# Optimization experiments

Measured on AMD Instinct MI355X. Metric: run time of the kernel, lower is better.

The kernel has to match this reference:

```python
import jax, jax.numpy as jnp
import numpy as np

B, S, F_IN, H, P2 = 64, 64, 2048, 512, 20  # batch, seq_len, input_size, hidden, 2*num_prototype


def setup_inputs() -> dict:
    key = jax.random.key(0)
    ks = jax.random.split(key, 16)
    sc = 0.02
    inp = {
        "v_feat": jax.random.normal(ks[0], (B, S, F_IN), jnp.float32),
        "category": jax.random.randint(ks[1], (B,), 0, 3, jnp.int64),
        "W_enc": jax.random.normal(ks[2], (F_IN, H), jnp.float32) * sc,
        "b_enc": jnp.zeros((H,), jnp.float32),
        # gate order along last axis: input, forget, output, memory(g)
        "Wx": jax.random.normal(ks[3], (H, 4 * H), jnp.float32) * sc,
        "bx": jnp.zeros((4 * H,), jnp.float32),
        "Wh": jax.random.normal(ks[4], (H, 4 * H), jnp.float32) * sc,
        "bh": jnp.zeros((4 * H,), jnp.float32),
        "cat_emb": jax.random.normal(ks[5], (3, H), jnp.float32) * sc,
        "W_dec": jax.random.normal(ks[6], (H, 1), jnp.float32) * sc,
        "b_dec": jnp.zeros((1,), jnp.float32),
        "prototype": jax.random.uniform(ks[7], (P2, F_IN), jnp.float32),
        "W_dd": jax.random.normal(ks[8], (P2 * S, 1), jnp.float32) * sc,
        "b_dd": jnp.zeros((1,), jnp.float32),
        "W_gate": jax.random.normal(ks[9], (F_IN, 1), jnp.float32) * sc,
        "b_gate": jnp.zeros((1,), jnp.float32),
    }
    return inp


def _forward(v_feat, category, W_enc, b_enc, Wx, bx, Wh, bh, cat_emb,
             W_dec, b_dec, prototype, W_dd, b_dd, W_gate, b_gate):
    batch, seq, feat = v_feat.shape
    # encoder + category fusion
    fuse = jax.nn.relu(jnp.einsum('bsf,fh->bsh', v_feat, W_enc) + b_enc)
    fuse = fuse + cat_emb[category][:, None, :]

    # fused-gate LSTM over time (note: original cell has NO tanh on cell in h = o*c)
    x_gates = jnp.einsum('bsh,hg->sbg', fuse, Wx) + (bx + bh)  # precompute input GEMM

    def step(carry, xg):
        h, c = carry
        gates = xg + h @ Wh
        i, f, o, g = jnp.split(gates, 4, axis=-1)
        i, f, o = jax.nn.sigmoid(i), jax.nn.sigmoid(f), jax.nn.sigmoid(o)
        g = jnp.tanh(g)
        c = f * c + i * g
        h = o * c
        return (h, c), None

    h0 = jnp.zeros((batch, Wh.shape[0]), fuse.dtype)
    (h, c), _ = jax.lax.scan(step, (h0, h0), x_gates)

    # dropout p=0.5 omitted (deterministic eval reference)
    output = jax.nn.sigmoid(h @ W_dec + b_dec)  # [B,1]

    # prototype distances: [B,S,2P]
    diff = v_feat[:, :, None, :] - prototype[None, None, :, :]
    dist = jnp.sum(diff * diff, axis=-1)
    dist_feat = jnp.log((dist + 1.0) / (dist + 1e-8))
    dist_pred = jax.nn.sigmoid(dist_feat.reshape(batch, -1) @ W_dd + b_dd)
    gate = jax.nn.sigmoid(jnp.mean(v_feat, axis=1) @ W_gate + b_gate)
    return output * gate + dist_pred * (1.0 - gate)


def reference(v_feat, category, W_enc, b_enc, Wx, bx, Wh, bh, cat_emb,
              W_dec, b_dec, prototype, W_dd, b_dd, W_gate, b_gate):
    return _forward(v_feat, category, W_enc, b_enc, Wx, bx, Wh, bh, cat_emb,
                    W_dec, b_dec, prototype, W_dd, b_dd, W_gate, b_gate)
```

## Files before the change

kernel.cpp:

```cpp
#include <hip/hip_runtime.h>
#include <cstdint>
#include <cstddef>


typedef __attribute__((ext_vector_type(8))) short short8;
typedef __attribute__((ext_vector_type(4))) float f32x4;
typedef unsigned long long ull;

__device__ __forceinline__ ushort f2bf(float x) {
    uint32_t u = __float_as_uint(x);
    return (ushort)((u + 0x7FFF + ((u >> 16) & 1)) >> 16);
}
__device__ __forceinline__ float bf2f(ushort u) {
    return __uint_as_float(((uint32_t)u) << 16);
}
__device__ __forceinline__ float sigm(float x) { return 1.f / (1.f + expf(-x)); }
__device__ __forceinline__ float tanh_fast(float x) { return 2.f / (1.f + expf(-2.f * x)) - 1.f; }

__global__ __launch_bounds__(256) void k_prep(
    const float* __restrict__ v_feat, const float* __restrict__ proto,
    const float* __restrict__ bx, const float* __restrict__ bh,
    const float* __restrict__ W_enc, const float* __restrict__ Wx,
    const float* __restrict__ Wh, const float* __restrict__ W_gate,
    ushort* __restrict__ v_bf16, ushort* __restrict__ proto_bf,
    float* __restrict__ bxh, ushort* __restrict__ Wenc_t,
    ushort* __restrict__ Wx_t, ushort* __restrict__ Whr,
    float* __restrict__ n2, float* __restrict__ gpart, float* __restrict__ p2,
    ushort* __restrict__ hbuf, int* __restrict__ flags, int* __restrict__ dd_done,
    int* __restrict__ xgf)
{
    __shared__ float ts[32][33];
    const int blk = blockIdx.x;
    const int tid = threadIdx.x;

    if (blk < 4096) {
        const int bs = blk;
        const float* vr = v_feat + (size_t)bs * 2048;
        float4 x0 = ((const float4*)vr)[tid];
        float4 x1 = ((const float4*)vr)[tid + 256];
        float4 w0 = ((const float4*)W_gate)[tid];
        float4 w1 = ((const float4*)W_gate)[tid + 256];
        ushort4 o0, o1;
        o0.x = f2bf(x0.x); o0.y = f2bf(x0.y); o0.z = f2bf(x0.z); o0.w = f2bf(x0.w);
        o1.x = f2bf(x1.x); o1.y = f2bf(x1.y); o1.z = f2bf(x1.z); o1.w = f2bf(x1.w);
        ((ushort4*)v_bf16)[(size_t)bs * 512 + tid] = o0;
        ((ushort4*)v_bf16)[(size_t)bs * 512 + tid + 256] = o1;
        float a = x0.x * x0.x + x0.y * x0.y + x0.z * x0.z + x0.w * x0.w
                + x1.x * x1.x + x1.y * x1.y + x1.z * x1.z + x1.w * x1.w;
        float g = x0.x * w0.x + x0.y * w0.y + x0.z * w0.z + x0.w * w0.w
                + x1.x * w1.x + x1.y * w1.y + x1.z * w1.z + x1.w * w1.w;
        const int lane = tid & 63, w = tid >> 6;
#pragma unroll
        for (int o = 32; o > 0; o >>= 1) { a += __shfl_down(a, o); g += __shfl_down(g, o); }
        if (lane == 0) { ts[0][w] = a; ts[1][w] = g; }
        __syncthreads();
        if (tid == 0) {
            n2[bs]    = ts[0][0] + ts[0][1] + ts[0][2] + ts[0][3];
            gpart[bs] = ts[1][0] + ts[1][1] + ts[1][2] + ts[1][3];
        }
    } else if (blk < 4136) {
        int i = (blk - 4096) * 256 + tid;
        float4 v = ((const float4*)proto)[i];
        ushort4 o;
        o.x = f2bf(v.x); o.y = f2bf(v.y); o.z = f2bf(v.z); o.w = f2bf(v.w);
        ((ushort4*)proto_bf)[i] = o;
    } else if (blk < 4148) {
        int row = 20 + (blk - 4136);
        ushort4 z = {0, 0, 0, 0};
        ((ushort4*)(proto_bf + (size_t)row * 2048))[tid * 2] = z;
        ((ushort4*)(proto_bf + (size_t)row * 2048))[tid * 2 + 1] = z;
    } else if (blk < 4156) {
        int n = (blk - 4148) * 256 + tid;
        int np = ((n & 511) << 2) | (n >> 9);
        bxh[np] = bx[n] + bh[n];
    } else if (blk < 7228) {
        const float* in;
        ushort* outp;
        int R, C, remap, t;
        if (blk < 5180)      { in = W_enc; outp = Wenc_t; R = 2048; C = 512;  remap = 0; t = blk - 4156; }
        else if (blk < 6204) { in = Wx;    outp = Wx_t;   R = 512;  C = 2048; remap = 1; t = blk - 5180; }
        else                 { in = Wh;    outp = Whr;    R = 512;  C = 2048; remap = 1; t = blk - 6204; }
        int tpr = C / 32;
        int cx = t % tpr, cy = t / tpr;
        int r0 = cy * 32, c0 = cx * 32;
        int rr = tid >> 3, cc = (tid & 7) * 4;
        float4 v = *(const float4*)(in + (size_t)(r0 + rr) * C + c0 + cc);
        ts[rr][cc + 0] = v.x; ts[rr][cc + 1] = v.y; ts[rr][cc + 2] = v.z; ts[rr][cc + 3] = v.w;
        __syncthreads();
        ushort4 o;
        o.x = f2bf(ts[cc + 0][rr]);
        o.y = f2bf(ts[cc + 1][rr]);
        o.z = f2bf(ts[cc + 2][rr]);
        o.w = f2bf(ts[cc + 3][rr]);
        int n = c0 + rr;
        int np = remap ? (((n & 511) << 2) | (n >> 9)) : n;
        *(ushort4*)(outp + (size_t)np * R + r0 + cc) = o;
    } else if (blk == 7228) {
        const int lane = tid & 63, w = tid >> 6;
        for (int p = w; p < 20; p += 4) {
            const float* pr = proto + (size_t)p * 2048;
            float a = 0.f;
#pragma unroll
            for (int i = 0; i < 8; ++i) {
                float4 x = ((const float4*)pr)[i * 64 + lane];
                a += x.x * x.x + x.y * x.y + x.z * x.z + x.w * x.w;
            }
#pragma unroll
            for (int o = 32; o > 0; o >>= 1) a += __shfl_down(a, o);
            if (lane == 0) p2[p] = a;
        }
        if (tid == 0) *dd_done = 0;
    } else if (blk < 7261) {
        ((ull*)hbuf)[(blk - 7229) * 256 + tid] = 0ULL;
    } else {
        for (int i = tid; i < 2048; i += 256) flags[i] = 0;
        for (int i = tid; i < 512; i += 256) xgf[i] = 0;
    }
}

__global__ __launch_bounds__(256) void k_mid(
    const ushort* __restrict__ A, const ushort* __restrict__ Bt,
    const float* __restrict__ bias0,
    const float* __restrict__ cat_emb, const int* __restrict__ category,
    ushort* __restrict__ C,
    const ushort* __restrict__ proto_bf, float* __restrict__ dots)
{
    __shared__ ushort As[64][40];
    __shared__ ushort Bs[128][40];
    const int tid = threadIdx.x;
    const int lane = tid & 63, w = tid >> 6;
    const int quad = lane >> 4, l16 = lane & 15;
    const int blk = blockIdx.x;

    if (blk >= 256) {
        const int r0 = (blk - 256) * 64 + w * 16;
        f32x4 acc[2] = {};
        const ushort* arow = A + (size_t)(r0 + l16) * 2048 + quad * 8;
        const ushort* b0p = proto_bf + (size_t)l16 * 2048 + quad * 8;
        const ushort* b1p = proto_bf + (size_t)(16 + l16) * 2048 + quad * 8;
#pragma unroll 8
        for (int kk = 0; kk < 64; ++kk) {
            short8 af = *(const short8*)(arow + kk * 32);
            short8 bf0 = *(const short8*)(b0p + kk * 32);
            short8 bf1 = *(const short8*)(b1p + kk * 32);
            acc[0] = __builtin_amdgcn_mfma_f32_16x16x32_bf16(af, bf0, acc[0], 0, 0, 0);
            acc[1] = __builtin_amdgcn_mfma_f32_16x16x32_bf16(af, bf1, acc[1], 0, 0, 0);
        }
#pragma unroll
        for (int t = 0; t < 2; ++t)
#pragma unroll
            for (int r = 0; r < 4; ++r)
                dots[(size_t)(r0 + quad * 4 + r) * 32 + t * 16 + l16] = acc[t][r];
        return;
    }

    const int m0 = (blk >> 2) * 64, n0 = (blk & 3) * 128;
    const int wm = (w & 1) * 32, wn = (w >> 1) * 64;
    const int K = 2048;

    f32x4 acc[2][4] = {};
    const int lr = tid >> 2;
    const int lc = (tid & 3) * 8;

    for (int k0 = 0; k0 < K; k0 += 32) {
        uint4 a0 = *(const uint4*)(A + (size_t)(m0 + lr) * K + k0 + lc);
        uint4 b0 = *(const uint4*)(Bt + (size_t)(n0 + lr) * K + k0 + lc);
        uint4 b1 = *(const uint4*)(Bt + (size_t)(n0 + 64 + lr) * K + k0 + lc);
        __syncthreads();
        *(uint4*)&As[lr][lc] = a0;
        *(uint4*)&Bs[lr][lc] = b0;
        *(uint4*)&Bs[64 + lr][lc] = b1;
        __syncthreads();
        short8 af[2], bf[4];
#pragma unroll
        for (int i = 0; i < 2; ++i) af[i] = *(const short8*)&As[wm + i * 16 + l16][quad * 8];
#pragma unroll
        for (int j = 0; j < 4; ++j) bf[j] = *(const short8*)&Bs[wn + j * 16 + l16][quad * 8];
#pragma unroll
        for (int i = 0; i < 2; ++i)
#pragma unroll
            for (int j = 0; j < 4; ++j)
                acc[i][j] = __builtin_amdgcn_mfma_f32_16x16x32_bf16(af[i], bf[j], acc[i][j], 0, 0, 0);
    }

#pragma unroll
    for (int i = 0; i < 2; ++i) {
        int mbase = m0 + wm + i * 16 + quad * 4;
#pragma unroll
        for (int r = 0; r < 4; ++r) {
            int m = mbase + r;
            const float* ce = cat_emb + category[m >> 6] * 512;
#pragma unroll
            for (int j = 0; j < 4; ++j) {
                int n = n0 + wn + j * 16 + l16;
                float v = fmaxf(acc[i][j][r] + bias0[n], 0.f) + ce[n];
                C[(size_t)m * 512 + n] = f2bf(v);
            }
        }
    }
}

__global__ __launch_bounds__(512, 2) void k_lstm_persist(
    ushort* __restrict__ xg,
    const ushort* __restrict__ fuse,
    const ushort* __restrict__ Wx_t,
    const float* __restrict__ bxh,
    int* __restrict__ xgf,
    const ushort* __restrict__ Whr,
    ushort* __restrict__ hbuf,
    int* __restrict__ flags,
    const float* __restrict__ W_dec, const float* __restrict__ b_dec,
    const float* __restrict__ b_dd, const float* __restrict__ b_gate,
    const float* __restrict__ dots, const float* __restrict__ n2,
    const float* __restrict__ p2, const float* __restrict__ W_dd,
    const float* __restrict__ gpart,
    float* __restrict__ dd_logit, float* __restrict__ g_logit,
    int* __restrict__ dd_done,
    float* __restrict__ out)
{
    __shared__ __align__(16) ushort hin_s[16 * 520];
    __shared__ __align__(16) ushort hstage[512];
    __shared__ float fred[8][64];
    __shared__ __align__(16) ushort As[128][40];
    __shared__ __align__(16) ushort Bs[128][40];

    const int tid = threadIdx.x;
    const int lane = tid & 63, wv = tid >> 6;
    const int quad = lane >> 4, l16 = lane & 15;
    const int bn = blockIdx.x;

    if (bn >= 320) {
        const int b = bn - 320;
        if (tid < 64) {
            float gp = gpart[b * 64 + tid];
#pragma unroll
            for (int o = 32; o > 0; o >>= 1) gp += __shfl_down(gp, o);
            if (tid == 0)
                __hip_atomic_store(&g_logit[b], gp, __ATOMIC_RELAXED, __HIP_MEMORY_SCOPE_AGENT);
        }
        float acc = 0.f;
        for (int u = tid; u < 1280; u += 512) {
            int s = u / 20, p = u - s * 20;
            int bs = b * 64 + s;
            float d = n2[bs] - 2.f * dots[(size_t)bs * 32 + p] + p2[p];
            acc += logf((d + 1.0f) / (d + 1e-8f)) * W_dd[s * 20 + p];
        }
#pragma unroll
        for (int o = 32; o > 0; o >>= 1) acc += __shfl_down(acc, o);
        if (lane == 0) fred[wv][0] = acc;
        __syncthreads();
        if (tid == 0) {
            float t = 0.f;
#pragma unroll
            for (int p = 0; p < 8; ++p) t += fred[p][0];
            __hip_atomic_store(&dd_logit[b], t, __ATOMIC_RELAXED, __HIP_MEMORY_SCOPE_AGENT);
            __hip_atomic_fetch_add(dd_done, 1, __ATOMIC_RELEASE, __HIP_MEMORY_SCOPE_AGENT);
        }
        return;
    }

    if (bn >= 64) {
        const int g = bn - 64;
        const int nc = g & 15;
        const int n0 = nc * 128;
        const int lrA = tid >> 2;
        const int lcA = (tid & 3) * 8;
        const int w8 = tid >> 6;
        const int wm8 = (w8 & 3) * 32, wn8 = (w8 >> 2) * 64;

#pragma unroll
        for (int ph = 0; ph < 2; ++ph) {
            const int mt = (ph ? 16 : 0) + (g >> 4);
            const int m0 = mt * 128;
            f32x4 acc[2][4] = {};
            for (int k0 = 0; k0 < 512; k0 += 32) {
                int ma = m0 + lrA;
                int fr = ((ma & 63) << 6) | (ma >> 6);
                uint4 a0 = *(const uint4*)(fuse + (size_t)fr * 512 + k0 + lcA);
                uint4 b0 = *(const uint4*)(Wx_t + (size_t)(n0 + lrA) * 512 + k0 + lcA);
                __syncthreads();
                *(uint4*)&As[lrA][lcA] = a0;
                *(uint4*)&Bs[lrA][lcA] = b0;
                __syncthreads();
                short8 af[2], bf[4];
#pragma unroll
                for (int i = 0; i < 2; ++i) af[i] = *(const short8*)&As[wm8 + i * 16 + l16][quad * 8];
#pragma unroll
                for (int j = 0; j < 4; ++j) bf[j] = *(const short8*)&Bs[wn8 + j * 16 + l16][quad * 8];
#pragma unroll
                for (int i = 0; i < 2; ++i)
#pragma unroll
                    for (int j = 0; j < 4; ++j)
                        acc[i][j] = __builtin_amdgcn_mfma_f32_16x16x32_bf16(af[i], bf[j], acc[i][j], 0, 0, 0);
            }
            float bb[4];
#pragma unroll
            for (int j = 0; j < 4; ++j) bb[j] = bxh[n0 + wn8 + j * 16 + l16];
#pragma unroll
            for (int i = 0; i < 2; ++i) {
                int mbase = m0 + wm8 + i * 16 + quad * 4;
#pragma unroll
                for (int r = 0; r < 4; ++r) {
                    ushort* crow = xg + (size_t)(mbase + r) * 2048;
#pragma unroll
                    for (int j = 0; j < 4; ++j)
                        crow[n0 + wn8 + j * 16 + l16] = f2bf(acc[i][j][r] + bb[j]);
                }
            }
            asm volatile("s_waitcnt vmcnt(0)" ::: "memory");
            __syncthreads();
            if (tid == 0)
                __hip_atomic_store(&xgf[mt * 16 + nc], 1, __ATOMIC_RELAXED,
                                   __HIP_MEMORY_SCOPE_AGENT);
        }
        return;
    }

    const int i = bn & 15;
    const int j = bn >> 4;
    const int uloc = wv * 4 + quad;

    short8 wfrag[16];
#pragma unroll
    for (int kc = 0; kc < 16; ++kc)
        wfrag[kc] = *(const short8*)(Whr +
            (size_t)(i * 128 + wv * 16 + l16) * 512 + kc * 32 + quad * 8);

    float c = 0.f;

    for (int s = 0; s < 64; ++s) {
        if (s > 0) {
            if (tid < 16) {
                const int* f = flags + (j * 16 + tid) * 32;
                while (__hip_atomic_load(f, __ATOMIC_RELAXED,
                                         __HIP_MEMORY_SCOPE_AGENT) < s) {}
            } else if (tid == 16) {
                const int xi = (s >> 1) * 16 + i;
                while (__hip_atomic_load(&xgf[xi], __ATOMIC_RELAXED,
                                         __HIP_MEMORY_SCOPE_AGENT) == 0) {}
            }
            __builtin_amdgcn_s_barrier();
            asm volatile("" ::: "memory");
        } else {
            if (tid == 0) {
                while (__hip_atomic_load(&xgf[i], __ATOMIC_RELAXED,
                                         __HIP_MEMORY_SCOPE_AGENT) == 0) {}
            }
            __builtin_amdgcn_s_barrier();
            asm volatile("" ::: "memory");
        }

        const ushort* xp = xg + (size_t)(s * 64 + j * 16 + l16) * 2048
                              + i * 128 + wv * 16 + quad * 4;
        ushort4 xa = *(const ushort4*)xp;

        const ushort* hin = hbuf + (size_t)s * 32768 + j * 8192;
        ushort* hout = hbuf + (size_t)(s + 1) * 32768 + j * 8192;

        {
            int r0 = wv * 2;
            __builtin_amdgcn_global_load_lds(
                (const __attribute__((address_space(1))) void*)(hin + (size_t)r0 * 512 + lane * 8),
                (__attribute__((address_space(3))) void*)(hin_s + r0 * 520),
                16, 0, 0);
            __builtin_amdgcn_global_load_lds(
                (const __attribute__((address_space(1))) void*)(hin + (size_t)(r0 + 1) * 512 + lane * 8),
                (__attribute__((address_space(3))) void*)(hin_s + (r0 + 1) * 520),
                16, 0, 0);
        }
        asm volatile("s_waitcnt vmcnt(0)" ::: "memory");
        __builtin_amdgcn_s_barrier();
        asm volatile("" ::: "memory");

        f32x4 aA = {bf2f(xa.x), bf2f(xa.y), bf2f(xa.z), bf2f(xa.w)};
        f32x4 aB = {};
#pragma unroll
        for (int kc = 0; kc < 16; kc += 2) {
            short8 h0 = *(const short8*)(hin_s + l16 * 520 + kc * 32 + quad * 8);
            short8 h1 = *(const short8*)(hin_s + l16 * 520 + (kc + 1) * 32 + quad * 8);
            aA = __builtin_amdgcn_mfma_f32_16x16x32_bf16(wfrag[kc], h0, aA, 0, 0, 0);
            aB = __builtin_amdgcn_mfma_f32_16x16x32_bf16(wfrag[kc + 1], h1, aB, 0, 0, 0);
        }

        float gi = sigm(aA[0] + aB[0]);
        float gf = sigm(aA[1] + aB[1]);
        float go = sigm(aA[2] + aB[2]);
        float gg = tanh_fast(aA[3] + aB[3]);
        c = gf * c + gi * gg;
        hstage[l16 * 32 + uloc] = f2bf(go * c);

        asm volatile("s_waitcnt lgkmcnt(0)" ::: "memory");
        __builtin_amdgcn_s_barrier();
        asm volatile("" ::: "memory");

        if (tid < 128) {
            int r = tid >> 3, ch = tid & 7;
            __hip_atomic_store((ull*)(hout + (size_t)r * 512 + i * 32) + ch,
                               ((const ull*)hstage)[tid],
                               __ATOMIC_RELAXED, __HIP_MEMORY_SCOPE_AGENT);
        }
        __syncthreads();
        if (tid == 0)
            __hip_atomic_store(&flags[bn * 32], s + 1, __ATOMIC_RELAXED,
                               __HIP_MEMORY_SCOPE_AGENT);
    }

    if (bn == 0) {
        if (tid < 64) {
            while (__hip_atomic_load(&flags[tid * 32], __ATOMIC_RELAXED,
                                     __HIP_MEMORY_SCOPE_AGENT) < 64) {}
        }
        __syncthreads();
        asm volatile("" ::: "memory");
        const ushort* hb64 = hbuf + (size_t)64 * 32768;
        int b = tid & 63, part = tid >> 6;
        const ushort* row = hb64 + (size_t)(b >> 4) * 8192 + (b & 15) * 512;
        float acc = 0.f;
#pragma unroll
        for (int g8 = 0; g8 < 8; ++g8) {
            const ushort* hp = row + part * 64 + g8 * 8;
            const float* wd = W_dec + part * 64 + g8 * 8;
#pragma unroll
            for (int half = 0; half < 2; ++half) {
                ull u = *(const ull*)(hp + half * 4);
                acc += bf2f((ushort)u) * wd[half * 4]
                     + bf2f((ushort)(u >> 16)) * wd[half * 4 + 1]
                     + bf2f((ushort)(u >> 32)) * wd[half * 4 + 2]
                     + bf2f((ushort)(u >> 48)) * wd[half * 4 + 3];
            }
        }
        fred[part][b] = acc;
        __syncthreads();
        if (tid == 0) {
            while (__hip_atomic_load(dd_done, __ATOMIC_RELAXED,
                                     __HIP_MEMORY_SCOPE_AGENT) < 64) {}
        }
        __syncthreads();
        asm volatile("" ::: "memory");
        if (tid < 64) {
            float a = 0.f;
#pragma unroll
            for (int p = 0; p < 8; ++p) a += fred[p][tid];
            float gl = __hip_atomic_load(&g_logit[tid], __ATOMIC_RELAXED,
                                         __HIP_MEMORY_SCOPE_AGENT);
            float dl = __hip_atomic_load(&dd_logit[tid], __ATOMIC_RELAXED,
                                         __HIP_MEMORY_SCOPE_AGENT);
            float output = sigm(a + b_dec[0]);
            float gate   = sigm(gl * (1.0f / 64.f) + b_gate[0]);
            float ddp    = sigm(dl + b_dd[0]);
            out[tid] = output * gate + ddp * (1.f - gate);
        }
    }
}

extern "C" void kernel_launch(void* const* d_in, const int* in_sizes, int n_in,
                              void* d_out, int out_size, void* d_ws, size_t ws_size,
                              hipStream_t stream) {
    const float* v_feat   = (const float*)d_in[0];
    const int*   category = (const int*)d_in[1];
    const float* W_enc    = (const float*)d_in[2];
    const float* b_enc    = (const float*)d_in[3];
    const float* Wx       = (const float*)d_in[4];
    const float* bx       = (const float*)d_in[5];
    const float* Wh       = (const float*)d_in[6];
    const float* bh       = (const float*)d_in[7];
    const float* cat_emb  = (const float*)d_in[8];
    const float* W_dec    = (const float*)d_in[9];
    const float* b_dec    = (const float*)d_in[10];
    const float* proto    = (const float*)d_in[11];
    const float* W_dd     = (const float*)d_in[12];
    const float* b_dd     = (const float*)d_in[13];
    const float* W_gate   = (const float*)d_in[14];
    const float* b_gate   = (const float*)d_in[15];
    float* out = (float*)d_out;

    char* ws = (char*)d_ws;
    ushort* xg       = (ushort*)(ws + 0);
    ushort* v_bf16   = (ushort*)(ws + 0);
    ushort* fuse     = (ushort*)(ws + 16777216);
    ushort* Whr      = (ushort*)(ws + 20971520);
    ushort* Wenc_t   = (ushort*)(ws + 23068672);
    ushort* Wx_t     = (ushort*)(ws + 25165824);
    ushort* proto_bf = (ushort*)(ws + 27262976);
    float*  dots     = (float*)(ws + 27394048);
    float*  n2       = (float*)(ws + 27918336);
    float*  gpart    = (float*)(ws + 27934720);
    float*  p2       = (float*)(ws + 27951104);
    int*    dd_done  = (int*)(ws + 27951232);
    float*  bxh      = (float*)(ws + 27951616);
    int*    flags    = (int*)(ws + 27959808);
    float*  dd_logit = (float*)(ws + 27967744);
    float*  g_logit  = (float*)(ws + 27968000);
    ushort* hbuf     = (ushort*)(ws + 27968256);
    int*    xgf      = (int*)(ws + 32228096);

    k_prep<<<7262, 256, 0, stream>>>(v_feat, proto, bx, bh, W_enc, Wx, Wh, W_gate,
                                     v_bf16, proto_bf, bxh, Wenc_t, Wx_t, Whr,
                                     n2, gpart, p2, hbuf, flags, dd_done, xgf);

    k_mid<<<320, 256, 0, stream>>>(v_bf16, Wenc_t, b_enc, cat_emb, category,
                                   fuse, proto_bf, dots);

    k_lstm_persist<<<384, 512, 0, stream>>>(xg, fuse, Wx_t, bxh, xgf,
                                            Whr, hbuf, flags,
                                            W_dec, b_dec, b_dd, b_gate,
                                            dots, n2, p2, W_dd, gpart,
                                            dd_logit, g_logit, dd_done, out);
}
```

Baseline: 231.9 us.

## Fuse v_feat bf16 conversion, norms and gate dot into the GEMM kernels

```diff
diff --git a/kernel.cpp b/kernel.cpp
--- a/kernel.cpp
+++ b/kernel.cpp
@@ -18,14 +18,14 @@
 __device__ __forceinline__ float tanh_fast(float x) { return 2.f / (1.f + expf(-2.f * x)) - 1.f; }
 
 __global__ __launch_bounds__(256) void k_prep(
-    const float* __restrict__ v_feat, const float* __restrict__ proto,
+    const float* __restrict__ proto,
     const float* __restrict__ bx, const float* __restrict__ bh,
     const float* __restrict__ W_enc, const float* __restrict__ Wx,
-    const float* __restrict__ Wh, const float* __restrict__ W_gate,
-    ushort* __restrict__ v_bf16, ushort* __restrict__ proto_bf,
+    const float* __restrict__ Wh,
+    ushort* __restrict__ proto_bf,
     float* __restrict__ bxh, ushort* __restrict__ Wenc_t,
     ushort* __restrict__ Wx_t, ushort* __restrict__ Whr,
-    float* __restrict__ n2, float* __restrict__ gpart, float* __restrict__ p2,
+    float* __restrict__ p2,
     ushort* __restrict__ hbuf, int* __restrict__ flags, int* __restrict__ dd_done,
     int* __restrict__ xgf)
 {
@@ -33,53 +33,28 @@
     const int blk = blockIdx.x;
     const int tid = threadIdx.x;
 
-    if (blk < 4096) {
-        const int bs = blk;
-        const float* vr = v_feat + (size_t)bs * 2048;
-        float4 x0 = ((const float4*)vr)[tid];
-        float4 x1 = ((const float4*)vr)[tid + 256];
-        float4 w0 = ((const float4*)W_gate)[tid];
-        float4 w1 = ((const float4*)W_gate)[tid + 256];
-        ushort4 o0, o1;
-        o0.x = f2bf(x0.x); o0.y = f2bf(x0.y); o0.z = f2bf(x0.z); o0.w = f2bf(x0.w);
-        o1.x = f2bf(x1.x); o1.y = f2bf(x1.y); o1.z = f2bf(x1.z); o1.w = f2bf(x1.w);
-        ((ushort4*)v_bf16)[(size_t)bs * 512 + tid] = o0;
-        ((ushort4*)v_bf16)[(size_t)bs * 512 + tid + 256] = o1;
-        float a = x0.x * x0.x + x0.y * x0.y + x0.z * x0.z + x0.w * x0.w
-                + x1.x * x1.x + x1.y * x1.y + x1.z * x1.z + x1.w * x1.w;
-        float g = x0.x * w0.x + x0.y * w0.y + x0.z * w0.z + x0.w * w0.w
-                + x1.x * w1.x + x1.y * w1.y + x1.z * w1.z + x1.w * w1.w;
-        const int lane = tid & 63, w = tid >> 6;
-#pragma unroll
-        for (int o = 32; o > 0; o >>= 1) { a += __shfl_down(a, o); g += __shfl_down(g, o); }
-        if (lane == 0) { ts[0][w] = a; ts[1][w] = g; }
-        __syncthreads();
-        if (tid == 0) {
-            n2[bs]    = ts[0][0] + ts[0][1] + ts[0][2] + ts[0][3];
-            gpart[bs] = ts[1][0] + ts[1][1] + ts[1][2] + ts[1][3];
-        }
-    } else if (blk < 4136) {
-        int i = (blk - 4096) * 256 + tid;
+    if (blk < 40) {
+        int i = blk * 256 + tid;
         float4 v = ((const float4*)proto)[i];
         ushort4 o;
         o.x = f2bf(v.x); o.y = f2bf(v.y); o.z = f2bf(v.z); o.w = f2bf(v.w);
         ((ushort4*)proto_bf)[i] = o;
-    } else if (blk < 4148) {
-        int row = 20 + (blk - 4136);
+    } else if (blk < 52) {
+        int row = 20 + (blk - 40);
         ushort4 z = {0, 0, 0, 0};
         ((ushort4*)(proto_bf + (size_t)row * 2048))[tid * 2] = z;
         ((ushort4*)(proto_bf + (size_t)row * 2048))[tid * 2 + 1] = z;
-    } else if (blk < 4156) {
-        int n = (blk - 4148) * 256 + tid;
+    } else if (blk < 60) {
+        int n = (blk - 52) * 256 + tid;
         int np = ((n & 511) << 2) | (n >> 9);
         bxh[np] = bx[n] + bh[n];
-    } else if (blk < 7228) {
+    } else if (blk < 3132) {
         const float* in;
         ushort* outp;
         int R, C, remap, t;
-        if (blk < 5180)      { in = W_enc; outp = Wenc_t; R = 2048; C = 512;  remap = 0; t = blk - 4156; }
-        else if (blk < 6204) { in = Wx;    outp = Wx_t;   R = 512;  C = 2048; remap = 1; t = blk - 5180; }
-        else                 { in = Wh;    outp = Whr;    R = 512;  C = 2048; remap = 1; t = blk - 6204; }
+        if (blk < 1084)      { in = W_enc; outp = Wenc_t; R = 2048; C = 512;  remap = 0; t = blk - 60; }
+        else if (blk < 2108) { in = Wx;    outp = Wx_t;   R = 512;  C = 2048; remap = 1; t = blk - 1084; }
+        else                 { in = Wh;    outp = Whr;    R = 512;  C = 2048; remap = 1; t = blk - 2108; }
         int tpr = C / 32;
         int cx = t % tpr, cy = t / tpr;
         int r0 = cy * 32, c0 = cx * 32;
@@ -95,7 +70,7 @@
         int n = c0 + rr;
         int np = remap ? (((n & 511) << 2) | (n >> 9)) : n;
         *(ushort4*)(outp + (size_t)np * R + r0 + cc) = o;
-    } else if (blk == 7228) {
+    } else if (blk == 3132) {
         const int lane = tid & 63, w = tid >> 6;
         for (int p = w; p < 20; p += 4) {
             const float* pr = proto + (size_t)p * 2048;
@@ -110,8 +85,8 @@
             if (lane == 0) p2[p] = a;
         }
         if (tid == 0) *dd_done = 0;
-    } else if (blk < 7261) {
-        ((ull*)hbuf)[(blk - 7229) * 256 + tid] = 0ULL;
+    } else if (blk < 3165) {
+        ((ull*)hbuf)[(blk - 3133) * 256 + tid] = 0ULL;
     } else {
         for (int i = tid; i < 2048; i += 256) flags[i] = 0;
         for (int i = tid; i < 512; i += 256) xgf[i] = 0;
@@ -119,11 +94,13 @@
 }
 
 __global__ __launch_bounds__(256) void k_mid(
-    const ushort* __restrict__ A, const ushort* __restrict__ Bt,
+    const float* __restrict__ v_feat, const ushort* __restrict__ Bt,
     const float* __restrict__ bias0,
     const float* __restrict__ cat_emb, const int* __restrict__ category,
     ushort* __restrict__ C,
-    const ushort* __restrict__ proto_bf, float* __restrict__ dots)
+    const ushort* __restrict__ proto_bf, float* __restrict__ dots,
+    const float* __restrict__ W_gate,
+    float* __restrict__ n2, float* __restrict__ gpart)
 {
     __shared__ ushort As[64][40];
     __shared__ ushort Bs[128][40];
@@ -135,12 +112,26 @@
     if (blk >= 256) {
         const int r0 = (blk - 256) * 64 + w * 16;
         f32x4 acc[2] = {};
-        const ushort* arow = A + (size_t)(r0 + l16) * 2048 + quad * 8;
+        const float* arow = v_feat + (size_t)(r0 + l16) * 2048 + quad * 8;
+        const float* wrow = W_gate + quad * 8;
         const ushort* b0p = proto_bf + (size_t)l16 * 2048 + quad * 8;
         const ushort* b1p = proto_bf + (size_t)(16 + l16) * 2048 + quad * 8;
-#pragma unroll 8
+        float sa = 0.f, sg = 0.f;
+#pragma unroll 4
         for (int kk = 0; kk < 64; ++kk) {
-            short8 af = *(const short8*)(arow + kk * 32);
+            float4 x0 = ((const float4*)(arow + kk * 32))[0];
+            float4 x1 = ((const float4*)(arow + kk * 32))[1];
+            float4 w0 = ((const float4*)(wrow + kk * 32))[0];
+            float4 w1 = ((const float4*)(wrow + kk * 32))[1];
+            short8 af;
+            af[0] = (short)f2bf(x0.x); af[1] = (short)f2bf(x0.y);
+            af[2] = (short)f2bf(x0.z); af[3] = (short)f2bf(x0.w);
+            af[4] = (short)f2bf(x1.x); af[5] = (short)f2bf(x1.y);
+            af[6] = (short)f2bf(x1.z); af[7] = (short)f2bf(x1.w);
+            sa += x0.x * x0.x + x0.y * x0.y + x0.z * x0.z + x0.w * x0.w
+                + x1.x * x1.x + x1.y * x1.y + x1.z * x1.z + x1.w * x1.w;
+            sg += x0.x * w0.x + x0.y * w0.y + x0.z * w0.z + x0.w * w0.w
+                + x1.x * w1.x + x1.y * w1.y + x1.z * w1.z + x1.w * w1.w;
             short8 bf0 = *(const short8*)(b0p + kk * 32);
             short8 bf1 = *(const short8*)(b1p + kk * 32);
             acc[0] = __builtin_amdgcn_mfma_f32_16x16x32_bf16(af, bf0, acc[0], 0, 0, 0);
@@ -151,6 +142,12 @@
 #pragma unroll
             for (int r = 0; r < 4; ++r)
                 dots[(size_t)(r0 + quad * 4 + r) * 32 + t * 16 + l16] = acc[t][r];
+        sa += __shfl_down(sa, 32); sa += __shfl_down(sa, 16);
+        sg += __shfl_down(sg, 32); sg += __shfl_down(sg, 16);
+        if (lane < 16) {
+            n2[r0 + lane] = sa;
+            gpart[r0 + lane] = sg;
+        }
         return;
     }
 
@@ -163,11 +160,17 @@
     const int lc = (tid & 3) * 8;
 
     for (int k0 = 0; k0 < K; k0 += 32) {
-        uint4 a0 = *(const uint4*)(A + (size_t)(m0 + lr) * K + k0 + lc);
+        const float* ap = v_feat + (size_t)(m0 + lr) * K + k0 + lc;
+        float4 va = ((const float4*)ap)[0];
+        float4 vb = ((const float4*)ap)[1];
         uint4 b0 = *(const uint4*)(Bt + (size_t)(n0 + lr) * K + k0 + lc);
         uint4 b1 = *(const uint4*)(Bt + (size_t)(n0 + 64 + lr) * K + k0 + lc);
-        __syncthreads();
-        *(uint4*)&As[lr][lc] = a0;
+        ushort4 ca, cb;
+        ca.x = f2bf(va.x); ca.y = f2bf(va.y); ca.z = f2bf(va.z); ca.w = f2bf(va.w);
+        cb.x = f2bf(vb.x); cb.y = f2bf(vb.y); cb.z = f2bf(vb.z); cb.w = f2bf(vb.w);
+        __syncthreads();
+        *(ushort4*)&As[lr][lc] = ca;
+        *(ushort4*)&As[lr][lc + 4] = cb;
         *(uint4*)&Bs[lr][lc] = b0;
         *(uint4*)&Bs[64 + lr][lc] = b1;
         __syncthreads();
@@ -316,6 +319,7 @@
         return;
     }
 
+    __builtin_amdgcn_s_setprio(1);
     const int i = bn & 15;
     const int j = bn >> 4;
     const int uloc = wv * 4 + quad;
@@ -476,7 +480,6 @@
 
     char* ws = (char*)d_ws;
     ushort* xg       = (ushort*)(ws + 0);
-    ushort* v_bf16   = (ushort*)(ws + 0);
     ushort* fuse     = (ushort*)(ws + 16777216);
     ushort* Whr      = (ushort*)(ws + 20971520);
     ushort* Wenc_t   = (ushort*)(ws + 23068672);
@@ -494,12 +497,12 @@
     ushort* hbuf     = (ushort*)(ws + 27968256);
     int*    xgf      = (int*)(ws + 32228096);
 
-    k_prep<<<7262, 256, 0, stream>>>(v_feat, proto, bx, bh, W_enc, Wx, Wh, W_gate,
-                                     v_bf16, proto_bf, bxh, Wenc_t, Wx_t, Whr,
-                                     n2, gpart, p2, hbuf, flags, dd_done, xgf);
-
-    k_mid<<<320, 256, 0, stream>>>(v_bf16, Wenc_t, b_enc, cat_emb, category,
-                                   fuse, proto_bf, dots);
+    k_prep<<<3166, 256, 0, stream>>>(proto, bx, bh, W_enc, Wx, Wh,
+                                     proto_bf, bxh, Wenc_t, Wx_t, Whr,
+                                     p2, hbuf, flags, dd_done, xgf);
+
+    k_mid<<<320, 256, 0, stream>>>(v_feat, Wenc_t, b_enc, cat_emb, category,
+                                   fuse, proto_bf, dots, W_gate, n2, gpart);
 
     k_lstm_persist<<<384, 512, 0, stream>>>(xg, fuse, Wx_t, bxh, xgf,
                                             Whr, hbuf, flags,
```

New measurement: 239.4 us. 3.2% more time.
